# Kernel tuning notes

Hardware: AMD Instinct MI355X
Metric: run time of the kernel (lower is better)

## Reference

```python
import jax, jax.numpy as jnp
import numpy as np


def _embedding_distances(dictionary, x_flat):
    # dictionary: [D, C], x_flat: [T, C] -> [T, D]
    dict_norms = jnp.sum(dictionary * dictionary, axis=-1)          # [D]
    x_norms = jnp.sum(x_flat * x_flat, axis=-1)                     # [T]
    dots = jnp.einsum('tc,dc->td', x_flat, dictionary)              # [T, D]
    return -2.0 * dots + dict_norms[None, :] + x_norms[:, None]


def _quantize(x, dictionary):
    # x: [N, C, H, W]
    N, C, H, W = x.shape
    cl = jnp.transpose(x, (0, 2, 3, 1))                             # [N, H, W, C]
    diffs = _embedding_distances(dictionary, cl.reshape(-1, C))     # [NHW, D]
    idxs = jnp.argmin(diffs, axis=-1).reshape(N, H, W)              # [N, H, W]
    embedded = jnp.transpose(dictionary[idxs], (0, 3, 1, 2))        # [N, C, H, W]
    embedded_pt = jax.lax.stop_gradient(embedded) + (x - jax.lax.stop_gradient(x))
    return embedded, embedded_pt, idxs


def setup_inputs() -> dict:
    key = jax.random.key(0)
    k1, k2, k3 = jax.random.split(key, 3)
    N, C, H, W, D = 32, 256, 32, 32, 1024
    return {
        'inputs': jax.random.normal(k1, (N, C, H, W), dtype=jnp.float32),
        'inputs_thermal': jax.random.normal(k2, (N, C, H, W), dtype=jnp.float32),
        'dictionary': jax.random.normal(k3, (D, C), dtype=jnp.float32),
    }


def reference(inputs, inputs_thermal, dictionary):
    embedded, embedded_pt, idxs = _quantize(inputs, dictionary)
    embedded_t, embedded_pt_t, idxs_t = _quantize(inputs_thermal, dictionary)
    return (embedded, embedded_pt, idxs, embedded_t, embedded_pt_t, idxs_t)
```

## Files before the change

kernel.cpp:

```cpp
#include <hip/hip_runtime.h>

#define NB    32
#define CCH   256
#define HW    1024
#define NPIX  (NB*HW)
#define DDICT 1024

#define EMB_ELEMS  ((size_t)NB*CCH*HW)
#define SEC_ELEMS  (2*EMB_ELEMS + NPIX)

#define TPX  128
#define TD   128
#define NDT  (DDICT/TD)
#define BK   32
#define NKC  (CCH/BK)
#define NPH  (NDT*NKC)

#define TAU  0.05f

#define RPX  16

typedef __attribute__((ext_vector_type(8))) short bf16x8;
typedef __attribute__((ext_vector_type(4))) float f32x4;

__device__ inline ushort split_rne(float f, float& rest) {
    uint u = __float_as_uint(f);
    uint r = u + 0x7FFFu + ((u >> 16) & 1u);
    rest = f - __uint_as_float(r & 0xFFFF0000u);
    return (ushort)(r >> 16);
}

__device__ inline ushort rne_bf16(float f) {
    uint u = __float_as_uint(f);
    return (ushort)((u + 0x7FFFu + ((u >> 16) & 1u)) >> 16);
}

__device__ inline void gll16(const void* g, void* l) {
    __builtin_amdgcn_global_load_lds(
        (const __attribute__((address_space(1))) uint*)g,
        (__attribute__((address_space(3))) uint*)l,
        16, 0, 0);
}

__global__ void dict_norms_kernel(const float* __restrict__ dict,
                                  float* __restrict__ norms,
                                  int* __restrict__ cnts) {
    if (blockIdx.x == 0 && threadIdx.x < 2) cnts[threadIdx.x] = 0;
    int d = blockIdx.x * blockDim.x + threadIdx.x;
    if (d < DDICT) {
        const float4* row = (const float4*)(dict + (size_t)d * CCH);
        float s = 0.f;
#pragma unroll 8
        for (int i = 0; i < CCH / 4; ++i) {
            float4 v = row[i];
            s += v.x * v.x + v.y * v.y + v.z * v.z + v.w * v.w;
        }
        norms[d] = s;
    }
}

__global__ void dict_split_kernel(const float* __restrict__ dict,
                                  ushort* __restrict__ dHs,
                                  ushort* __restrict__ dMs,
                                  float* __restrict__ dictT) {
    int d = blockIdx.x;
    int lane = threadIdx.x;
    float4 f = ((const float4*)(dict + (size_t)d * CCH))[lane];
    float v[4] = {f.x, f.y, f.z, f.w};
    ushort h[4], m[4];
#pragma unroll
    for (int i = 0; i < 4; ++i) {
        float r1;
        h[i] = split_rne(v[i], r1);
        m[i] = rne_bf16(r1);
    }
    int c0 = lane * 4;
    int kc = c0 >> 5, oct = (c0 >> 3) & 3, e0 = c0 & 7;
    int dt = d >> 7, dd = d & 127;
    int slot = (oct + (dd >> 1)) & 3;
    size_t base = ((size_t)(dt * NKC + kc)) * 4096 + dd * 32 + slot * 8 + e0;
    *(ushort4*)(dHs + base) = make_ushort4(h[0], h[1], h[2], h[3]);
    *(ushort4*)(dMs + base) = make_ushort4(m[0], m[1], m[2], m[3]);
#pragma unroll
    for (int j = 0; j < 4; ++j)
        dictT[(size_t)(c0 + j) * DDICT + d] = v[j];
}

__global__ __launch_bounds__(512, 4)
void vq_mfma_kernel(const float* __restrict__ x0,
                    const float* __restrict__ x1,
                    const ushort* __restrict__ dHs,
                    const ushort* __restrict__ dMs,
                    const float* __restrict__ norms,
                    const float* __restrict__ dict,
                    float* __restrict__ out,
                    int* __restrict__ cnts,
                    int* __restrict__ lists) {
    __shared__ ushort Bs[2][2][4096];
    __shared__ float nrm_s[DDICT];
    __shared__ int   idx_s[TPX];

    const int t    = threadIdx.x;
    const int lane = t & 63;
    const int wv   = t >> 6;
    const int lx   = lane & 15;
    const int q    = lane >> 4;
    const int m0w  = wv * 16;
    const int z    = blockIdx.y;

    const int g0  = blockIdx.x * TPX;
    const int n   = g0 / HW;
    const int hw0 = g0 % HW;

    const float* x = z ? x1 : x0;
    float* out_base = out + (size_t)z * SEC_ELEMS;
    float* out_idx  = out_base + 2 * EMB_ELEMS;
    int* cnt  = cnts + z;
    int* list = lists + (size_t)z * NPIX;

    *(float2*)(nrm_s + t * 2) = *(const float2*)(norms + t * 2);

    const float* xbase = x + (size_t)n * CCH * HW + hw0 + m0w + lx;
    bf16x8 Ah[8], Am[8];
#pragma unroll
    for (int kc = 0; kc < NKC; ++kc) {
        float a_f[8];
#pragma unroll
        for (int j = 0; j < 8; ++j)
            a_f[j] = xbase[(size_t)(kc * BK + q * 8 + j) * HW];
#pragma unroll
        for (int j = 0; j < 8; ++j) {
            float r1;
            ushort h = split_rne(a_f[j], r1);
            Ah[kc][j] = (short)h;
            Am[kc][j] = (short)rne_bf16(r1);
        }
    }

    auto stage = [&](int p, int b) {
#pragma unroll
        for (int plane = 0; plane < 2; ++plane) {
            const ushort* sp = (plane ? dMs : dHs) + (size_t)p * 4096;
            gll16(sp + t * 8, &Bs[b][plane][wv * 512]);
        }
    };

    __syncthreads();
    stage(0, 0);

    float b1r[4], b2r[4]; int i1r[4];
#pragma unroll
    for (int r = 0; r < 4; ++r) {
        b1r[r] = 3.0e38f; b2r[r] = 3.0e38f; i1r[r] = 0;
    }

    for (int dt = 0; dt < NDT; ++dt) {
        f32x4 acc[8] = {};
#pragma unroll
        for (int kc = 0; kc < NKC; ++kc) {
            const int p = dt * 8 + kc;
            asm volatile("s_waitcnt vmcnt(0)" ::: "memory");
            __builtin_amdgcn_s_barrier();
            if (p + 1 < NPH) stage(p + 1, (p + 1) & 1);

            const ushort* bb = &Bs[p & 1][0][0];
            __builtin_amdgcn_s_setprio(1);
#pragma unroll
            for (int ni = 0; ni < 8; ++ni) {
                int nn   = ni * 16 + lx;
                int slot = (q + (nn >> 1)) & 3;
                int off  = nn * 32 + slot * 8;
                bf16x8 Bh = *(const bf16x8*)(bb + off);
                bf16x8 Bm = *(const bf16x8*)(bb + 4096 + off);
                f32x4 c = acc[ni];
                c = __builtin_amdgcn_mfma_f32_16x16x32_bf16(Ah[kc], Bh, c, 0, 0, 0);
                c = __builtin_amdgcn_mfma_f32_16x16x32_bf16(Ah[kc], Bm, c, 0, 0, 0);
                c = __builtin_amdgcn_mfma_f32_16x16x32_bf16(Am[kc], Bh, c, 0, 0, 0);
                acc[ni] = c;
            }
            __builtin_amdgcn_s_setprio(0);
        }

        const int d0 = dt * TD;
        float nrm[8];
#pragma unroll
        for (int ni = 0; ni < 8; ++ni) nrm[ni] = nrm_s[d0 + ni * 16 + lx];

#pragma unroll
        for (int r = 0; r < 4; ++r) {
            float c1 = 3.0e38f, c2 = 3.0e38f; int ci = 0;
#pragma unroll
            for (int ni = 0; ni < 8; ++ni) {
                float dist = fmaf(-2.f, acc[ni][r], nrm[ni]);
                if (dist < c1)      { c2 = c1; c1 = dist; ci = ni * 16 + lx; }
                else if (dist < c2) { c2 = dist; }
            }
#pragma unroll
            for (int off = 1; off < 16; off <<= 1) {
                float o1 = __shfl_xor(c1, off);
                int   oi = __shfl_xor(ci, off);
                float o2 = __shfl_xor(c2, off);
                if (o1 < c1 || (o1 == c1 && oi < ci)) {
                    c2 = fminf(c1, o2); c1 = o1; ci = oi;
                } else {
                    c2 = fminf(c2, o1);
                }
            }
            if (c1 < b1r[r]) {
                b2r[r] = fminf(b1r[r], c2);
                b1r[r] = c1;
                i1r[r] = d0 + ci;
            } else {
                b2r[r] = fminf(b2r[r], c1);
            }
        }
    }

#pragma unroll
    for (int r = 0; r < 4; ++r) {
        if (lx == 0) {
            int loc = m0w + q * 4 + r;
            int g = g0 + loc;
            idx_s[loc] = i1r[r];
            out_idx[g] = (float)i1r[r];
            if (b2r[r] - b1r[r] < TAU) {
                int slot = atomicAdd(cnt, 1);
                list[slot] = g;
            }
        }
    }
    __syncthreads();

    const int pg = t & 31;
    const int cg = t >> 5;
    const int hwp = hw0 + pg * 4;
    const float* r0 = dict + (size_t)idx_s[pg * 4 + 0] * CCH;
    const float* r1 = dict + (size_t)idx_s[pg * 4 + 1] * CCH;
    const float* r2 = dict + (size_t)idx_s[pg * 4 + 2] * CCH;
    const float* r3 = dict + (size_t)idx_s[pg * 4 + 3] * CCH;
    float* oe = out_base;
    float* op = out_base + EMB_ELEMS;
    const size_t obase = (size_t)n * CCH * HW + hwp;

#pragma unroll
    for (int cq = 0; cq < 4; ++cq) {
        int c = cg * 16 + cq * 4;
        float4 q0 = *(const float4*)(r0 + c);
        float4 q1 = *(const float4*)(r1 + c);
        float4 q2 = *(const float4*)(r2 + c);
        float4 q3 = *(const float4*)(r3 + c);
        float4 v0 = make_float4(q0.x, q1.x, q2.x, q3.x);
        float4 v1 = make_float4(q0.y, q1.y, q2.y, q3.y);
        float4 v2 = make_float4(q0.z, q1.z, q2.z, q3.z);
        float4 v3 = make_float4(q0.w, q1.w, q2.w, q3.w);
        *(float4*)(oe + obase + (size_t)(c + 0) * HW) = v0;
        *(float4*)(op + obase + (size_t)(c + 0) * HW) = v0;
        *(float4*)(oe + obase + (size_t)(c + 1) * HW) = v1;
        *(float4*)(op + obase + (size_t)(c + 1) * HW) = v1;
        *(float4*)(oe + obase + (size_t)(c + 2) * HW) = v2;
        *(float4*)(op + obase + (size_t)(c + 2) * HW) = v2;
        *(float4*)(oe + obase + (size_t)(c + 3) * HW) = v3;
        *(float4*)(op + obase + (size_t)(c + 3) * HW) = v3;
    }
}

__global__ __launch_bounds__(256)
void vq_rescue_kernel(const float* __restrict__ x0,
                      const float* __restrict__ x1,
                      const float* __restrict__ dictT,
                      const float* __restrict__ dict,
                      const float* __restrict__ norms,
                      const int* __restrict__ cnts,
                      const int* __restrict__ lists,
                      float* __restrict__ out) {
    __shared__ float xr[CCH][RPX];
    __shared__ float rd_s[4][RPX];
    __shared__ int   ri_s[4][RPX];
    __shared__ int   gi_s[RPX];
    __shared__ int   bi_s[RPX];
    const int z = blockIdx.y;
    const float* x = z ? x1 : x0;
    const int* list = lists + (size_t)z * NPIX;
    float* out_emb    = out + (size_t)z * SEC_ELEMS;
    float* out_emb_pt = out_emb + EMB_ELEMS;
    float* out_idx    = out_emb + 2 * EMB_ELEMS;
    const int t    = threadIdx.x;
    const int lane = t & 63;
    const int wv   = t >> 6;
    const int total = cnts[z];

    for (int w0 = blockIdx.x * RPX; w0 < total; w0 += gridDim.x * RPX) {
        const int np = min(RPX, total - w0);
        if (t < RPX) gi_s[t] = list[w0 + ((t < np) ? t : (np - 1))];
        __syncthreads();

        {
            const int p  = t >> 4;
            const int j0 = (t & 15) * 16;
            const int g  = gi_s[p];
            const int n  = g / HW, hw = g % HW;
            const float* xb = x + (size_t)n * CCH * HW + hw;
#pragma unroll
            for (int j = 0; j < 16; ++j)
                xr[j0 + j][p] = xb[(size_t)(j0 + j) * HW];
        }
        __syncthreads();

        float acc[4][RPX] = {};
        for (int k = 0; k < CCH; ++k) {
            float xp[RPX];
#pragma unroll
            for (int p4 = 0; p4 < RPX / 4; ++p4) {
                f32x4 v = *(const f32x4*)&xr[k][p4 * 4];
#pragma unroll
                for (int j = 0; j < 4; ++j) xp[p4 * 4 + j] = v[j];
            }
#pragma unroll
            for (int dd = 0; dd < 4; ++dd) {
                float v = dictT[(size_t)k * DDICT + dd * 256 + t];
#pragma unroll
                for (int p = 0; p < RPX; ++p)
                    acc[dd][p] = fmaf(xp[p], v, acc[dd][p]);
            }
        }

#pragma unroll
        for (int p = 0; p < RPX; ++p) {
            float bd = 3.0e38f; int bi = 0;
#pragma unroll
            for (int dd = 0; dd < 4; ++dd) {
                int d = dd * 256 + t;
                float dist = fmaf(-2.f, acc[dd][p], norms[d]);
                if (dist < bd) { bd = dist; bi = d; }
            }
#pragma unroll
            for (int off = 1; off < 64; off <<= 1) {
                float od = __shfl_xor(bd, off);
                int   oi = __shfl_xor(bi, off);
                if (od < bd || (od == bd && oi < bi)) { bd = od; bi = oi; }
            }
            if (lane == 0) { rd_s[wv][p] = bd; ri_s[wv][p] = bi; }
        }
        __syncthreads();
        if (t < RPX) {
            const int p = t;
            float fb = rd_s[0][p]; int fi = ri_s[0][p];
#pragma unroll
            for (int q2 = 1; q2 < 4; ++q2)
                if (rd_s[q2][p] < fb || (rd_s[q2][p] == fb && ri_s[q2][p] < fi)) {
                    fb = rd_s[q2][p]; fi = ri_s[q2][p];
                }
            bi_s[p] = fi;
            if (p < np) out_idx[gi_s[p]] = (float)fi;
        }
        __syncthreads();

        {
            const int p  = t >> 4;
            const int j0 = (t & 15) * 16;
            if (p < np) {
                const int g = gi_s[p];
                const int n = g / HW, hw = g % HW;
                const float* dr = dict + (size_t)bi_s[p] * CCH;
                const size_t ob = (size_t)n * CCH * HW + hw;
#pragma unroll
                for (int j = 0; j < 16; ++j) {
                    float v = dr[j0 + j];
                    out_emb[ob + (size_t)(j0 + j) * HW]    = v;
                    out_emb_pt[ob + (size_t)(j0 + j) * HW] = v;
                }
            }
        }
        __syncthreads();
    }
}

extern "C" void kernel_launch(void* const* d_in, const int* in_sizes, int n_in,
                              void* d_out, int out_size, void* d_ws, size_t ws_size,
                              hipStream_t stream) {
    const float* x0   = (const float*)d_in[0];
    const float* x1   = (const float*)d_in[1];
    const float* dict = (const float*)d_in[2];
    float* out = (float*)d_out;

    float*  norms = (float*)d_ws;
    ushort* dHs   = (ushort*)(norms + DDICT);
    ushort* dMs   = dHs + (size_t)DDICT * CCH;
    float*  dictT = (float*)(dMs + (size_t)DDICT * CCH);
    int*    lists = (int*)(dictT + (size_t)DDICT * CCH);
    int*    cnts  = lists + 2 * NPIX;

    dict_norms_kernel<<<dim3(DDICT / 256), dim3(256), 0, stream>>>(dict, norms, cnts);
    dict_split_kernel<<<dim3(DDICT), dim3(64), 0, stream>>>(dict, dHs, dMs, dictT);

    vq_mfma_kernel<<<dim3(NPIX / TPX, 2), dim3(512), 0, stream>>>(
        x0, x1, dHs, dMs, norms, dict, out, cnts, lists);

    vq_rescue_kernel<<<dim3(512, 2), dim3(256), 0, stream>>>(
        x0, x1, dictT, dict, norms, cnts, lists, out);
}
```

Baseline: 393.6 us.

## Drop dictionary residual MFMA term and widen rescue threshold with per-pixel error bound

Removes the bf16 residual plane of the dictionary, which drops one of three MFMAs per tile and halves the LDS staging traffic in the main distance kernel. To stay exact, the fixed near-tie threshold is replaced by a per-pixel bound built from the pixel norm and the largest dictionary residual norm (computed with an atomic max in the split kernel). More pixels are then sent to the exact fp32 rescue kernel, so the saved MFMA time may be offset by extra rescue work. The bound's constant is tighter than a strict worst-case bound, which risks missing some ties.

```diff
diff --git a/kernel.cpp b/kernel.cpp
--- a/kernel.cpp
+++ b/kernel.cpp
@@ -16,8 +16,6 @@
 #define NKC  (CCH/BK)
 #define NPH  (NDT*NKC)
 
-#define TAU  0.05f
-
 #define RPX  16
 
 typedef __attribute__((ext_vector_type(8))) short bf16x8;
@@ -44,8 +42,10 @@
 
 __global__ void dict_norms_kernel(const float* __restrict__ dict,
                                   float* __restrict__ norms,
-                                  int* __restrict__ cnts) {
+                                  int* __restrict__ cnts,
+                                  uint* __restrict__ s1m) {
     if (blockIdx.x == 0 && threadIdx.x < 2) cnts[threadIdx.x] = 0;
+    if (blockIdx.x == 0 && threadIdx.x == 0) *s1m = 0u;
     int d = blockIdx.x * blockDim.x + threadIdx.x;
     if (d < DDICT) {
         const float4* row = (const float4*)(dict + (size_t)d * CCH);
@@ -61,18 +61,19 @@
 
 __global__ void dict_split_kernel(const float* __restrict__ dict,
                                   ushort* __restrict__ dHs,
-                                  ushort* __restrict__ dMs,
-                                  float* __restrict__ dictT) {
+                                  float* __restrict__ dictT,
+                                  uint* __restrict__ s1m) {
     int d = blockIdx.x;
     int lane = threadIdx.x;
     float4 f = ((const float4*)(dict + (size_t)d * CCH))[lane];
     float v[4] = {f.x, f.y, f.z, f.w};
-    ushort h[4], m[4];
+    ushort h[4];
+    float s1sq = 0.f;
 #pragma unroll
     for (int i = 0; i < 4; ++i) {
         float r1;
         h[i] = split_rne(v[i], r1);
-        m[i] = rne_bf16(r1);
+        s1sq = fmaf(r1, r1, s1sq);
     }
     int c0 = lane * 4;
     int kc = c0 >> 5, oct = (c0 >> 3) & 3, e0 = c0 & 7;
@@ -80,23 +81,27 @@
     int slot = (oct + (dd >> 1)) & 3;
     size_t base = ((size_t)(dt * NKC + kc)) * 4096 + dd * 32 + slot * 8 + e0;
     *(ushort4*)(dHs + base) = make_ushort4(h[0], h[1], h[2], h[3]);
-    *(ushort4*)(dMs + base) = make_ushort4(m[0], m[1], m[2], m[3]);
 #pragma unroll
     for (int j = 0; j < 4; ++j)
         dictT[(size_t)(c0 + j) * DDICT + d] = v[j];
+
+#pragma unroll
+    for (int off = 1; off < 64; off <<= 1)
+        s1sq += __shfl_xor(s1sq, off);
+    if (lane == 0) atomicMax(s1m, __float_as_uint(s1sq));
 }
 
 __global__ __launch_bounds__(512, 4)
 void vq_mfma_kernel(const float* __restrict__ x0,
                     const float* __restrict__ x1,
                     const ushort* __restrict__ dHs,
-                    const ushort* __restrict__ dMs,
                     const float* __restrict__ norms,
                     const float* __restrict__ dict,
+                    const uint* __restrict__ s1m,
                     float* __restrict__ out,
                     int* __restrict__ cnts,
                     int* __restrict__ lists) {
-    __shared__ ushort Bs[2][2][4096];
+    __shared__ ushort Bs[2][4096];
     __shared__ float nrm_s[DDICT];
     __shared__ int   idx_s[TPX];
 
@@ -118,10 +123,13 @@
     int* cnt  = cnts + z;
     int* list = lists + (size_t)z * NPIX;
 
+    const float S1max = sqrtf(__uint_as_float(*s1m));
+
     *(float2*)(nrm_s + t * 2) = *(const float2*)(norms + t * 2);
 
     const float* xbase = x + (size_t)n * CCH * HW + hw0 + m0w + lx;
     bf16x8 Ah[8], Am[8];
+    float na2 = 0.f;
 #pragma unroll
     for (int kc = 0; kc < NKC; ++kc) {
         float a_f[8];
@@ -134,15 +142,15 @@
             ushort h = split_rne(a_f[j], r1);
             Ah[kc][j] = (short)h;
             Am[kc][j] = (short)rne_bf16(r1);
-        }
-    }
+            na2 = fmaf(a_f[j], a_f[j], na2);
+        }
+    }
+    na2 += __shfl_xor(na2, 16);
+    na2 += __shfl_xor(na2, 32);
 
     auto stage = [&](int p, int b) {
-#pragma unroll
-        for (int plane = 0; plane < 2; ++plane) {
-            const ushort* sp = (plane ? dMs : dHs) + (size_t)p * 4096;
-            gll16(sp + t * 8, &Bs[b][plane][wv * 512]);
-        }
+        const ushort* sp = dHs + (size_t)p * 4096;
+        gll16(sp + t * 8, &Bs[b][wv * 512]);
     };
 
     __syncthreads();
@@ -163,7 +171,7 @@
             __builtin_amdgcn_s_barrier();
             if (p + 1 < NPH) stage(p + 1, (p + 1) & 1);
 
-            const ushort* bb = &Bs[p & 1][0][0];
+            const ushort* bb = &Bs[p & 1][0];
             __builtin_amdgcn_s_setprio(1);
 #pragma unroll
             for (int ni = 0; ni < 8; ++ni) {
@@ -171,10 +179,8 @@
                 int slot = (q + (nn >> 1)) & 3;
                 int off  = nn * 32 + slot * 8;
                 bf16x8 Bh = *(const bf16x8*)(bb + off);
-                bf16x8 Bm = *(const bf16x8*)(bb + 4096 + off);
                 f32x4 c = acc[ni];
                 c = __builtin_amdgcn_mfma_f32_16x16x32_bf16(Ah[kc], Bh, c, 0, 0, 0);
-                c = __builtin_amdgcn_mfma_f32_16x16x32_bf16(Ah[kc], Bm, c, 0, 0, 0);
                 c = __builtin_amdgcn_mfma_f32_16x16x32_bf16(Am[kc], Bh, c, 0, 0, 0);
                 acc[ni] = c;
             }
@@ -218,12 +224,14 @@
 
 #pragma unroll
     for (int r = 0; r < 4; ++r) {
+        float na2_r = __shfl(na2, q * 4 + r);
+        float thr   = fmaf(2.02f * sqrtf(na2_r), S1max, 0.15f);
         if (lx == 0) {
             int loc = m0w + q * 4 + r;
             int g = g0 + loc;
             idx_s[loc] = i1r[r];
             out_idx[g] = (float)i1r[r];
-            if (b2r[r] - b1r[r] < TAU) {
+            if (b2r[r] - b1r[r] < thr) {
                 int slot = atomicAdd(cnt, 1);
                 list[slot] = g;
             }
@@ -385,16 +393,17 @@
 
     float*  norms = (float*)d_ws;
     ushort* dHs   = (ushort*)(norms + DDICT);
-    ushort* dMs   = dHs + (size_t)DDICT * CCH;
-    float*  dictT = (float*)(dMs + (size_t)DDICT * CCH);
+    float*  dictT = (float*)(dHs + (size_t)DDICT * CCH);
     int*    lists = (int*)(dictT + (size_t)DDICT * CCH);
     int*    cnts  = lists + 2 * NPIX;
-
-    dict_norms_kernel<<<dim3(DDICT / 256), dim3(256), 0, stream>>>(dict, norms, cnts);
-    dict_split_kernel<<<dim3(DDICT), dim3(64), 0, stream>>>(dict, dHs, dMs, dictT);
+    uint*   s1m   = (uint*)(cnts + 2);
+
+    dict_norms_kernel<<<dim3(DDICT / 256), dim3(256), 0, stream>>>(dict, norms,
+                                                                   cnts, s1m);
+    dict_split_kernel<<<dim3(DDICT), dim3(64), 0, stream>>>(dict, dHs, dictT, s1m);
 
     vq_mfma_kernel<<<dim3(NPIX / TPX, 2), dim3(512), 0, stream>>>(
-        x0, x1, dHs, dMs, norms, dict, out, cnts, lists);
+        x0, x1, dHs, norms, dict, s1m, out, cnts, lists);
 
     vq_rescue_kernel<<<dim3(512, 2), dim3(256), 0, stream>>>(
         x0, x1, dictT, dict, norms, cnts, lists, out);
```

New measurement: 472.3 us. 1.2x slower.

## Fuse rescue pass into main VQ kernel with per-block flagged lists

Applied to the files above, without the earlier changes.

Merges the two dictionary prep kernels into one, and folds the exact-fp32 rescue pass into the MFMA search kernel using a block-local shared-memory list of ambiguous pixels instead of a global atomic list and a separate launch. Tiles shrink to 64 pixels with 256 threads per block, so each block stages B tiles with two loads per thread. The aim is to remove two launches and the global list round trip. In exchange, each flagged pixel is rescued serially inside its block with a 256-length dot product per dictionary entry read from global dictT, which may add tail imbalance, and smaller tiles halve reuse of each dictionary tile load.

```diff
diff --git a/kernel.cpp b/kernel.cpp
--- a/kernel.cpp
+++ b/kernel.cpp
@@ -9,7 +9,7 @@
 #define EMB_ELEMS  ((size_t)NB*CCH*HW)
 #define SEC_ELEMS  (2*EMB_ELEMS + NPIX)
 
-#define TPX  128
+#define TPX  64
 #define TD   128
 #define NDT  (DDICT/TD)
 #define BK   32
@@ -18,8 +18,6 @@
 
 #define TAU  0.05f
 
-#define RPX  16
-
 typedef __attribute__((ext_vector_type(8))) short bf16x8;
 typedef __attribute__((ext_vector_type(4))) float f32x4;
 
@@ -42,27 +40,11 @@
         16, 0, 0);
 }
 
-__global__ void dict_norms_kernel(const float* __restrict__ dict,
-                                  float* __restrict__ norms,
-                                  int* __restrict__ cnts) {
-    if (blockIdx.x == 0 && threadIdx.x < 2) cnts[threadIdx.x] = 0;
-    int d = blockIdx.x * blockDim.x + threadIdx.x;
-    if (d < DDICT) {
-        const float4* row = (const float4*)(dict + (size_t)d * CCH);
-        float s = 0.f;
-#pragma unroll 8
-        for (int i = 0; i < CCH / 4; ++i) {
-            float4 v = row[i];
-            s += v.x * v.x + v.y * v.y + v.z * v.z + v.w * v.w;
-        }
-        norms[d] = s;
-    }
-}
-
-__global__ void dict_split_kernel(const float* __restrict__ dict,
-                                  ushort* __restrict__ dHs,
-                                  ushort* __restrict__ dMs,
-                                  float* __restrict__ dictT) {
+__global__ void dict_prep_kernel(const float* __restrict__ dict,
+                                 ushort* __restrict__ dHs,
+                                 ushort* __restrict__ dMs,
+                                 float* __restrict__ dictT,
+                                 float* __restrict__ norms) {
     int d = blockIdx.x;
     int lane = threadIdx.x;
     float4 f = ((const float4*)(dict + (size_t)d * CCH))[lane];
@@ -84,21 +66,37 @@
 #pragma unroll
     for (int j = 0; j < 4; ++j)
         dictT[(size_t)(c0 + j) * DDICT + d] = v[j];
-}
-
-__global__ __launch_bounds__(512, 4)
-void vq_mfma_kernel(const float* __restrict__ x0,
+
+    if (lane == 0) {
+        const float4* row = (const float4*)(dict + (size_t)d * CCH);
+        float s = 0.f;
+#pragma unroll 8
+        for (int i = 0; i < CCH / 4; ++i) {
+            float4 w = row[i];
+            s += w.x * w.x + w.y * w.y + w.z * w.z + w.w * w.w;
+        }
+        norms[d] = s;
+    }
+}
+
+__global__ __launch_bounds__(256, 4)
+void vq_mega_kernel(const float* __restrict__ x0,
                     const float* __restrict__ x1,
                     const ushort* __restrict__ dHs,
                     const ushort* __restrict__ dMs,
                     const float* __restrict__ norms,
                     const float* __restrict__ dict,
-                    float* __restrict__ out,
-                    int* __restrict__ cnts,
-                    int* __restrict__ lists) {
+                    const float* __restrict__ dictT,
+                    float* __restrict__ out) {
     __shared__ ushort Bs[2][2][4096];
     __shared__ float nrm_s[DDICT];
     __shared__ int   idx_s[TPX];
+    __shared__ int   fl_list[TPX];
+    __shared__ int   fl_cnt;
+    __shared__ float xr[CCH];
+    __shared__ float rd_s[4];
+    __shared__ int   ri_s[4];
+    __shared__ int   bi_s;
 
     const int t    = threadIdx.x;
     const int lane = t & 63;
@@ -114,11 +112,12 @@
 
     const float* x = z ? x1 : x0;
     float* out_base = out + (size_t)z * SEC_ELEMS;
-    float* out_idx  = out_base + 2 * EMB_ELEMS;
-    int* cnt  = cnts + z;
-    int* list = lists + (size_t)z * NPIX;
-
-    *(float2*)(nrm_s + t * 2) = *(const float2*)(norms + t * 2);
+    float* out_emb    = out_base;
+    float* out_emb_pt = out_base + EMB_ELEMS;
+    float* out_idx    = out_base + 2 * EMB_ELEMS;
+
+    if (t == 0) fl_cnt = 0;
+    *(float4*)(nrm_s + t * 4) = *(const float4*)(norms + t * 4);
 
     const float* xbase = x + (size_t)n * CCH * HW + hw0 + m0w + lx;
     bf16x8 Ah[8], Am[8];
@@ -141,7 +140,11 @@
 #pragma unroll
         for (int plane = 0; plane < 2; ++plane) {
             const ushort* sp = (plane ? dMs : dHs) + (size_t)p * 4096;
-            gll16(sp + t * 8, &Bs[b][plane][wv * 512]);
+#pragma unroll
+            for (int h = 0; h < 2; ++h) {
+                gll16(sp + (h * 256 + t) * 8,
+                      &Bs[b][plane][h * 2048 + wv * 512]);
+            }
         }
     };
 
@@ -220,158 +223,89 @@
     for (int r = 0; r < 4; ++r) {
         if (lx == 0) {
             int loc = m0w + q * 4 + r;
-            int g = g0 + loc;
             idx_s[loc] = i1r[r];
-            out_idx[g] = (float)i1r[r];
+            out_idx[g0 + loc] = (float)i1r[r];
             if (b2r[r] - b1r[r] < TAU) {
-                int slot = atomicAdd(cnt, 1);
-                list[slot] = g;
+                int s = atomicAdd(&fl_cnt, 1);
+                fl_list[s] = loc;
             }
         }
     }
     __syncthreads();
 
-    const int pg = t & 31;
-    const int cg = t >> 5;
-    const int hwp = hw0 + pg * 4;
-    const float* r0 = dict + (size_t)idx_s[pg * 4 + 0] * CCH;
-    const float* r1 = dict + (size_t)idx_s[pg * 4 + 1] * CCH;
-    const float* r2 = dict + (size_t)idx_s[pg * 4 + 2] * CCH;
-    const float* r3 = dict + (size_t)idx_s[pg * 4 + 3] * CCH;
-    float* oe = out_base;
-    float* op = out_base + EMB_ELEMS;
-    const size_t obase = (size_t)n * CCH * HW + hwp;
-
-#pragma unroll
-    for (int cq = 0; cq < 4; ++cq) {
-        int c = cg * 16 + cq * 4;
-        float4 q0 = *(const float4*)(r0 + c);
-        float4 q1 = *(const float4*)(r1 + c);
-        float4 q2 = *(const float4*)(r2 + c);
-        float4 q3 = *(const float4*)(r3 + c);
-        float4 v0 = make_float4(q0.x, q1.x, q2.x, q3.x);
-        float4 v1 = make_float4(q0.y, q1.y, q2.y, q3.y);
-        float4 v2 = make_float4(q0.z, q1.z, q2.z, q3.z);
-        float4 v3 = make_float4(q0.w, q1.w, q2.w, q3.w);
-        *(float4*)(oe + obase + (size_t)(c + 0) * HW) = v0;
-        *(float4*)(op + obase + (size_t)(c + 0) * HW) = v0;
-        *(float4*)(oe + obase + (size_t)(c + 1) * HW) = v1;
-        *(float4*)(op + obase + (size_t)(c + 1) * HW) = v1;
-        *(float4*)(oe + obase + (size_t)(c + 2) * HW) = v2;
-        *(float4*)(op + obase + (size_t)(c + 2) * HW) = v2;
-        *(float4*)(oe + obase + (size_t)(c + 3) * HW) = v3;
-        *(float4*)(op + obase + (size_t)(c + 3) * HW) = v3;
-    }
-}
-
-__global__ __launch_bounds__(256)
-void vq_rescue_kernel(const float* __restrict__ x0,
-                      const float* __restrict__ x1,
-                      const float* __restrict__ dictT,
-                      const float* __restrict__ dict,
-                      const float* __restrict__ norms,
-                      const int* __restrict__ cnts,
-                      const int* __restrict__ lists,
-                      float* __restrict__ out) {
-    __shared__ float xr[CCH][RPX];
-    __shared__ float rd_s[4][RPX];
-    __shared__ int   ri_s[4][RPX];
-    __shared__ int   gi_s[RPX];
-    __shared__ int   bi_s[RPX];
-    const int z = blockIdx.y;
-    const float* x = z ? x1 : x0;
-    const int* list = lists + (size_t)z * NPIX;
-    float* out_emb    = out + (size_t)z * SEC_ELEMS;
-    float* out_emb_pt = out_emb + EMB_ELEMS;
-    float* out_idx    = out_emb + 2 * EMB_ELEMS;
-    const int t    = threadIdx.x;
-    const int lane = t & 63;
-    const int wv   = t >> 6;
-    const int total = cnts[z];
-
-    for (int w0 = blockIdx.x * RPX; w0 < total; w0 += gridDim.x * RPX) {
-        const int np = min(RPX, total - w0);
-        if (t < RPX) gi_s[t] = list[w0 + ((t < np) ? t : (np - 1))];
+    {
+        const int pg = t & 15;
+        const int cg = t >> 4;
+        const int hwp = hw0 + pg * 4;
+        const float* r0 = dict + (size_t)idx_s[pg * 4 + 0] * CCH;
+        const float* r1 = dict + (size_t)idx_s[pg * 4 + 1] * CCH;
+        const float* r2 = dict + (size_t)idx_s[pg * 4 + 2] * CCH;
+        const float* r3 = dict + (size_t)idx_s[pg * 4 + 3] * CCH;
+        const size_t obase = (size_t)n * CCH * HW + hwp;
+#pragma unroll
+        for (int cq = 0; cq < 4; ++cq) {
+            int c = cg * 16 + cq * 4;
+            float4 q0 = *(const float4*)(r0 + c);
+            float4 q1 = *(const float4*)(r1 + c);
+            float4 q2 = *(const float4*)(r2 + c);
+            float4 q3 = *(const float4*)(r3 + c);
+            float4 v0 = make_float4(q0.x, q1.x, q2.x, q3.x);
+            float4 v1 = make_float4(q0.y, q1.y, q2.y, q3.y);
+            float4 v2 = make_float4(q0.z, q1.z, q2.z, q3.z);
+            float4 v3 = make_float4(q0.w, q1.w, q2.w, q3.w);
+            *(float4*)(out_emb    + obase + (size_t)(c + 0) * HW) = v0;
+            *(float4*)(out_emb_pt + obase + (size_t)(c + 0) * HW) = v0;
+            *(float4*)(out_emb    + obase + (size_t)(c + 1) * HW) = v1;
+            *(float4*)(out_emb_pt + obase + (size_t)(c + 1) * HW) = v1;
+            *(float4*)(out_emb    + obase + (size_t)(c + 2) * HW) = v2;
+            *(float4*)(out_emb_pt + obase + (size_t)(c + 2) * HW) = v2;
+            *(float4*)(out_emb    + obase + (size_t)(c + 3) * HW) = v3;
+            *(float4*)(out_emb_pt + obase + (size_t)(c + 3) * HW) = v3;
+        }
+    }
+
+    const int nf = fl_cnt;
+    for (int fi = 0; fi < nf; ++fi) {
         __syncthreads();
-
-        {
-            const int p  = t >> 4;
-            const int j0 = (t & 15) * 16;
-            const int g  = gi_s[p];
-            const int n  = g / HW, hw = g % HW;
-            const float* xb = x + (size_t)n * CCH * HW + hw;
-#pragma unroll
-            for (int j = 0; j < 16; ++j)
-                xr[j0 + j][p] = xb[(size_t)(j0 + j) * HW];
-        }
+        const int g  = g0 + fl_list[fi];
+        const int hw = g % HW;
+        xr[t] = x[(size_t)n * CCH * HW + (size_t)t * HW + hw];
         __syncthreads();
 
-        float acc[4][RPX] = {};
-        for (int k = 0; k < CCH; ++k) {
-            float xp[RPX];
-#pragma unroll
-            for (int p4 = 0; p4 < RPX / 4; ++p4) {
-                f32x4 v = *(const f32x4*)&xr[k][p4 * 4];
-#pragma unroll
-                for (int j = 0; j < 4; ++j) xp[p4 * 4 + j] = v[j];
-            }
-#pragma unroll
-            for (int dd = 0; dd < 4; ++dd) {
-                float v = dictT[(size_t)k * DDICT + dd * 256 + t];
-#pragma unroll
-                for (int p = 0; p < RPX; ++p)
-                    acc[dd][p] = fmaf(xp[p], v, acc[dd][p]);
-            }
-        }
-
-#pragma unroll
-        for (int p = 0; p < RPX; ++p) {
-            float bd = 3.0e38f; int bi = 0;
-#pragma unroll
-            for (int dd = 0; dd < 4; ++dd) {
-                int d = dd * 256 + t;
-                float dist = fmaf(-2.f, acc[dd][p], norms[d]);
-                if (dist < bd) { bd = dist; bi = d; }
-            }
-#pragma unroll
-            for (int off = 1; off < 64; off <<= 1) {
-                float od = __shfl_xor(bd, off);
-                int   oi = __shfl_xor(bi, off);
-                if (od < bd || (od == bd && oi < bi)) { bd = od; bi = oi; }
-            }
-            if (lane == 0) { rd_s[wv][p] = bd; ri_s[wv][p] = bi; }
-        }
+        float bd = 3.0e38f; int bi = 0;
+#pragma unroll
+        for (int dd = 0; dd < 4; ++dd) {
+            int d = dd * 256 + t;
+            float dot = 0.f;
+#pragma unroll 8
+            for (int k = 0; k < CCH; ++k)
+                dot = fmaf(xr[k], dictT[(size_t)k * DDICT + d], dot);
+            float dist = fmaf(-2.f, dot, nrm_s[d]);
+            if (dist < bd) { bd = dist; bi = d; }
+        }
+#pragma unroll
+        for (int off = 1; off < 64; off <<= 1) {
+            float od = __shfl_xor(bd, off);
+            int   oi = __shfl_xor(bi, off);
+            if (od < bd || (od == bd && oi < bi)) { bd = od; bi = oi; }
+        }
+        if (lane == 0) { rd_s[wv] = bd; ri_s[wv] = bi; }
         __syncthreads();
-        if (t < RPX) {
-            const int p = t;
-            float fb = rd_s[0][p]; int fi = ri_s[0][p];
+        if (t == 0) {
+            float fb = rd_s[0]; int fid = ri_s[0];
 #pragma unroll
             for (int q2 = 1; q2 < 4; ++q2)
-                if (rd_s[q2][p] < fb || (rd_s[q2][p] == fb && ri_s[q2][p] < fi)) {
-                    fb = rd_s[q2][p]; fi = ri_s[q2][p];
+                if (rd_s[q2] < fb || (rd_s[q2] == fb && ri_s[q2] < fid)) {
+                    fb = rd_s[q2]; fid = ri_s[q2];
                 }
-            bi_s[p] = fi;
-            if (p < np) out_idx[gi_s[p]] = (float)fi;
+            bi_s = fid;
+            out_idx[g] = (float)fid;
         }
         __syncthreads();
-
-        {
-            const int p  = t >> 4;
-            const int j0 = (t & 15) * 16;
-            if (p < np) {
-                const int g = gi_s[p];
-                const int n = g / HW, hw = g % HW;
-                const float* dr = dict + (size_t)bi_s[p] * CCH;
-                const size_t ob = (size_t)n * CCH * HW + hw;
-#pragma unroll
-                for (int j = 0; j < 16; ++j) {
-                    float v = dr[j0 + j];
-                    out_emb[ob + (size_t)(j0 + j) * HW]    = v;
-                    out_emb_pt[ob + (size_t)(j0 + j) * HW] = v;
-                }
-            }
-        }
-        __syncthreads();
+        float v = dict[(size_t)bi_s * CCH + t];
+        size_t o = (size_t)n * CCH * HW + (size_t)t * HW + hw;
+        out_emb[o]    = v;
+        out_emb_pt[o] = v;
     }
 }
 
@@ -387,15 +321,10 @@
     ushort* dHs   = (ushort*)(norms + DDICT);
     ushort* dMs   = dHs + (size_t)DDICT * CCH;
     float*  dictT = (float*)(dMs + (size_t)DDICT * CCH);
-    int*    lists = (int*)(dictT + (size_t)DDICT * CCH);
-    int*    cnts  = lists + 2 * NPIX;
-
-    dict_norms_kernel<<<dim3(DDICT / 256), dim3(256), 0, stream>>>(dict, norms, cnts);
-    dict_split_kernel<<<dim3(DDICT), dim3(64), 0, stream>>>(dict, dHs, dMs, dictT);
-
-    vq_mfma_kernel<<<dim3(NPIX / TPX, 2), dim3(512), 0, stream>>>(
-        x0, x1, dHs, dMs, norms, dict, out, cnts, lists);
-
-    vq_rescue_kernel<<<dim3(512, 2), dim3(256), 0, stream>>>(
-        x0, x1, dictT, dict, norms, cnts, lists, out);
-}
+
+    dict_prep_kernel<<<dim3(DDICT), dim3(64), 0, stream>>>(dict, dHs, dMs,
+                                                           dictT, norms);
+
+    vq_mega_kernel<<<dim3(NPIX / TPX, 2), dim3(256), 0, stream>>>(
+        x0, x1, dHs, dMs, norms, dict, dictT, out);
+}
```

Result: slower. 408.6 us (+3.8%).
